# Kernel optimization log

Hardware: AMD Instinct MI355X
Metric: run time of the kernel (lower is better)

## Reference

```python
import jax, jax.numpy as jnp
import numpy as np

NUM_HEADS = 8
KERNEL = 7
LOW_RANK = 4


def setup_inputs() -> dict:
    key = jax.random.key(0)
    ks = jax.random.split(key, 10)
    B, H, W, C = 4, 56, 56, 256
    nh, K, lr = NUM_HEADS, KERNEL, LOW_RANK
    s = 0.02
    return {
        "x": jax.random.normal(ks[0], (B, H, W, C), jnp.float32),
        "Wq": jax.random.normal(ks[1], (C, nh * lr), jnp.float32) * s,
        "bq": jnp.zeros((nh * lr,), jnp.float32),
        "Wk": jax.random.normal(ks[2], (C, nh * lr), jnp.float32) * s,
        "bk": jnp.zeros((nh * lr,), jnp.float32),
        "Wv": jax.random.normal(ks[3], (C, C), jnp.float32) * s,
        "bv": jnp.zeros((C,), jnp.float32),
        "rpb": jax.random.normal(ks[4], (nh, 2 * K - 1, 2 * K - 1), jnp.float32) * s,
        "Wp": jax.random.normal(ks[5], (C, C), jnp.float32) * s,
        "bp": jnp.zeros((C,), jnp.float32),
    }


def reference(x, Wq, bq, Wk, bk, Wv, bv, rpb, Wp, bp):
    B, H, W, C = x.shape
    nh, K, lr = NUM_HEADS, KERNEL, LOW_RANK
    hd = C // nh
    r = K // 2
    scale = hd ** -0.5

    # Projections. Note: the original uses a raw reshape (B,H,W,nh*lr)->(B,nh,H,W,lr),
    # which we replicate exactly (row-major reshape, no permute).
    q = (x @ Wq + bq).reshape(B, nh, H, W, lr) * scale
    k = (x @ Wk + bk).reshape(B, nh, H, W, lr)
    v = (x @ Wv + bv).reshape(B, nh, H, W, hd)

    # NATTEN window start indices (clamped so each query sees exactly K keys per axis).
    start_h = jnp.clip(jnp.arange(H) - r, 0, H - K)  # (H,)
    start_w = jnp.clip(jnp.arange(W) - r, 0, W - K)  # (W,)
    idx_h = start_h[:, None] + jnp.arange(K)[None, :]  # (H, K)
    idx_w = start_w[:, None] + jnp.arange(K)[None, :]  # (W, K)

    # Gather local K/V windows: (B, nh, H, K, W, K, d)
    k_win = k[:, :, idx_h][:, :, :, :, idx_w]
    v_win = v[:, :, idx_h][:, :, :, :, idx_w]

    # Scores: (B, nh, H, W, K, K)
    attn = jnp.einsum('bhijc,bhikjlc->bhijkl', q, k_win)

    # Relative position bias indices: (key_pos - query_pos) + (K-1)
    bi = idx_h - jnp.arange(H)[:, None] + (K - 1)  # (H, K)
    bj = idx_w - jnp.arange(W)[:, None] + (K - 1)  # (W, K)
    bias = rpb[:, bi][:, :, :, bj]                 # (nh, H, K, W, K)
    attn = attn + bias.transpose(0, 1, 3, 2, 4)[None]  # (B, nh, H, W, K, K)

    attn = jax.nn.softmax(attn.reshape(B, nh, H, W, K * K), axis=-1)
    attn = attn.reshape(B, nh, H, W, K, K)

    # Weighted aggregation of V windows: (B, nh, H, W, hd)
    out = jnp.einsum('bhijkl,bhikjld->bhijd', attn, v_win)
    out = out.transpose(0, 2, 3, 1, 4).reshape(B, H, W, C)
    return out @ Wp + bp
```

## Files before the change

### kernel.cpp

```cpp
#include <hip/hip_runtime.h>
#include <hip/hip_bf16.h>

#define BD 4
#define HD_ 56
#define WD 56
#define CD 256
#define NH 8
#define KW 7
#define LR 4
#define HDIM 32
#define MB (HD_*WD)
#define NROWS (BD*MB)
#define QK_PER_B (HD_*WD*32)
#define V_PER_B  (HD_*WD*256)

typedef short short8 __attribute__((ext_vector_type(8)));
typedef float floatx4 __attribute__((ext_vector_type(4)));

static __device__ inline ushort f2bf(float f) {
    __hip_bfloat16 h = __float2bfloat16(f);
    return *(ushort*)&h;
}
static __device__ inline float bf2f(uint h16) {
    union { uint u; float f; } c; c.u = h16 << 16; return c.f;
}
static __device__ inline float bf2f_hi(uint u) {
    union { uint v; float f; } c; c.v = u & 0xffff0000u; return c.f;
}

__global__ __launch_bounds__(256) void prep_all(
    const float* __restrict__ x,
    const float* __restrict__ Wq, const float* __restrict__ Wk,
    const float* __restrict__ Wv, const float* __restrict__ bq,
    const float* __restrict__ bk, const float* __restrict__ bv,
    const float* __restrict__ Wp,
    ushort* __restrict__ Xb, ushort* __restrict__ WpkT,
    ushort* __restrict__ WpT, float* __restrict__ pb)
{
    int blk = blockIdx.x;
    if (blk < 1568) {
        int i8 = (blk * 256 + threadIdx.x) * 8;
        float4 u = *(const float4*)&x[i8];
        float4 v = *(const float4*)&x[i8 + 4];
        union { ushort h[8]; uint4 q; } pk;
        pk.h[0] = f2bf(u.x); pk.h[1] = f2bf(u.y); pk.h[2] = f2bf(u.z); pk.h[3] = f2bf(u.w);
        pk.h[4] = f2bf(v.x); pk.h[5] = f2bf(v.y); pk.h[6] = f2bf(v.z); pk.h[7] = f2bf(v.w);
        *(uint4*)&Xb[i8] = pk.q;
    } else {
        int idx = (blk - 1568) * 256 + threadIdx.x;
        if (idx < 81920) {
            int n = idx >> 8, k = idx & 255;
            float v;
            if (n < 32)       v = Wq[k * 32 + n];
            else if (n < 64)  v = Wk[k * 32 + (n - 32)];
            else              v = Wv[k * 256 + (n - 64)];
            WpkT[idx] = f2bf(v);
        } else if (idx < 81920 + 65536) {
            int j = idx - 81920;
            int n = j >> 8, k = j & 255;
            WpT[j] = f2bf(Wp[k * 256 + n]);
        } else if (idx < 81920 + 65536 + 320) {
            int n = idx - (81920 + 65536);
            pb[n] = (n < 32) ? bq[n] : (n < 64) ? bk[n - 32] : bv[n - 64];
        }
    }
}

__global__ __launch_bounds__(256) void mfma_qkv(
    const ushort* __restrict__ Ag, const ushort* __restrict__ Bt,
    const float* __restrict__ pb, ushort* __restrict__ Qb,
    ushort* __restrict__ Kb, ushort* __restrict__ Vb)
{
    __shared__ ushort As[64 * 40];
    __shared__ ushort Bs[64 * 40];

    const int t = threadIdx.x;
    const int m0 = blockIdx.y * 64;
    const int n0 = blockIdx.x * 64;
    const int r  = t >> 2;
    const int kq = (t & 3) << 3;
    const int lane = t & 63, w = t >> 6;
    const int col = lane & 15, quad = lane >> 4;
    const int q8 = quad << 3;

    floatx4 acc[4] = {{0,0,0,0},{0,0,0,0},{0,0,0,0},{0,0,0,0}};

    for (int k0 = 0; k0 < 256; k0 += 32) {
        uint4 av = *(const uint4*)&Ag[(m0 + r) * 256 + k0 + kq];
        uint4 bv = *(const uint4*)&Bt[(n0 + r) * 256 + k0 + kq];
        __syncthreads();
        *(uint4*)&As[r * 40 + kq] = av;
        *(uint4*)&Bs[r * 40 + kq] = bv;
        __syncthreads();
        short8 af = *(short8*)&As[((w << 4) + col) * 40 + q8];
#pragma unroll
        for (int nt = 0; nt < 4; ++nt) {
            short8 bf = *(short8*)&Bs[((nt << 4) + col) * 40 + q8];
            acc[nt] = __builtin_amdgcn_mfma_f32_16x16x32_bf16(af, bf, acc[nt], 0, 0, 0);
        }
    }

#pragma unroll
    for (int nt = 0; nt < 4; ++nt) {
        int gn = n0 + (nt << 4) + col;
        float bias = pb[gn];
#pragma unroll
        for (int rg = 0; rg < 4; ++rg) {
            int m = m0 + (w << 4) + (quad << 2) + rg;
            ushort h = f2bf(acc[nt][rg] + bias);
            if (n0 == 0 && nt < 2)      Qb[m * 32 + gn] = h;
            else if (n0 == 0)           Kb[m * 32 + (gn - 32)] = h;
            else                        Vb[m * 256 + (gn - 64)] = h;
        }
    }
}

__global__ __launch_bounds__(256) void mfma_out(
    const ushort* __restrict__ Ag, const ushort* __restrict__ Bt,
    const float* __restrict__ bp, float* __restrict__ out)
{
    __shared__ ushort As[64 * 40];
    __shared__ ushort Bs[64 * 40];

    const int t = threadIdx.x;
    const int m0 = blockIdx.y * 64;
    const int n0 = blockIdx.x * 64;
    const int r  = t >> 2;
    const int kq = (t & 3) << 3;
    const int lane = t & 63, w = t >> 6;
    const int col = lane & 15, quad = lane >> 4;
    const int q8 = quad << 3;

    floatx4 acc[4] = {{0,0,0,0},{0,0,0,0},{0,0,0,0},{0,0,0,0}};

    for (int k0 = 0; k0 < 256; k0 += 32) {
        uint4 av = *(const uint4*)&Ag[(m0 + r) * 256 + k0 + kq];
        uint4 bv = *(const uint4*)&Bt[(n0 + r) * 256 + k0 + kq];
        __syncthreads();
        *(uint4*)&As[r * 40 + kq] = av;
        *(uint4*)&Bs[r * 40 + kq] = bv;
        __syncthreads();
        short8 af = *(short8*)&As[((w << 4) + col) * 40 + q8];
#pragma unroll
        for (int nt = 0; nt < 4; ++nt) {
            short8 bf = *(short8*)&Bs[((nt << 4) + col) * 40 + q8];
            acc[nt] = __builtin_amdgcn_mfma_f32_16x16x32_bf16(af, bf, acc[nt], 0, 0, 0);
        }
    }

#pragma unroll
    for (int nt = 0; nt < 4; ++nt) {
        int gn = n0 + (nt << 4) + col;
        float bias = bp[gn];
#pragma unroll
        for (int rg = 0; rg < 4; ++rg) {
            int m = m0 + (w << 4) + (quad << 2) + rg;
            out[m * 256 + gn] = acc[nt][rg] + bias;
        }
    }
}

__global__ __launch_bounds__(256, 8) void natten_attn_t(
    const ushort* __restrict__ Qb, const ushort* __restrict__ Kb,
    const ushort* __restrict__ Vb, const float* __restrict__ rpb,
    ushort* __restrict__ Ab)
{
    __shared__ ushort Ks[196 * 4];
    __shared__ ushort Vs[4 * 196 * 8];
    __shared__ float  Rs[169];

    const int tj = blockIdx.x, ti = blockIdx.y;
    const int n = blockIdx.z & 7, b = blockIdx.z >> 3;
    const int t = threadIdx.x;
    const int i0 = ti * 8, j0 = tj * 8;
    const int rs = min(max(i0 - 3, 0), HD_ - 14);
    const int cs = min(max(j0 - 3, 0), WD - 14);

    const ushort* kb = Kb + b * QK_PER_B + n * (HD_ * WD * LR);
    const ushort* vb = Vb + b * V_PER_B + n * (HD_ * WD * HDIM);

    if (t < 196) {
        int r = t / 14, c = t % 14;
        *(uint2*)&Ks[t * 4] = *(const uint2*)&kb[(rs + r) * (WD * LR) + (cs + c) * LR];
    }
    if (t < 169) Rs[t] = rpb[n * 169 + t];
    for (int idx = t; idx < 784; idx += 256) {
        int oct = idx & 3, pos = idx >> 2;
        int r = pos / 14, c = pos % 14;
        *(uint4*)&Vs[(oct * 196 + pos) * 8] =
            *(const uint4*)&vb[(rs + r) * (WD * HDIM) + (cs + c) * HDIM + oct * 8];
    }
    __syncthreads();

    const int q  = t >> 2, p = t & 3;
    const int qi = q >> 3, qj = q & 7;
    const int i = i0 + qi, j = j0 + qj;
    const int sh = min(max(i - 3, 0), HD_ - KW);
    const int sw = min(max(j - 3, 0), WD - KW);
    const int oh = sh - rs, ow = sw - cs;

    union { uint2 u; uint w[2]; } qr;
    qr.u = *(const uint2*)&Qb[b * QK_PER_B + n * (HD_ * WD * LR) + i * (WD * LR) + j * LR];
    const float scale = 0.17677669529663687f;
    float qx = bf2f(qr.w[0] & 0xffff) * scale, qy = bf2f_hi(qr.w[0]) * scale;
    float qz = bf2f(qr.w[1] & 0xffff) * scale, qw = bf2f_hi(qr.w[1]) * scale;

    const int rb0 = (sh - i + 6) * 13 + (sw - j + 6);

    float mx = -3.4e38f;
    for (int kh = 0; kh < KW; ++kh) {
        int kpos  = (oh + kh) * 14 + ow;
        int rbase = rb0 + kh * 13;
#pragma unroll
        for (int kw = 0; kw < KW; ++kw) {
            union { uint2 u; uint w[2]; } kr;
            kr.u = *(const uint2*)&Ks[(kpos + kw) * 4];
            float d = Rs[rbase + kw];
            d = fmaf(qx, bf2f(kr.w[0] & 0xffff), d);
            d = fmaf(qy, bf2f_hi(kr.w[0]), d);
            d = fmaf(qz, bf2f(kr.w[1] & 0xffff), d);
            d = fmaf(qw, bf2f_hi(kr.w[1]), d);
            mx = fmaxf(mx, d);
        }
    }

    float sum = 0.f;
    float a[8] = {0.f, 0.f, 0.f, 0.f, 0.f, 0.f, 0.f, 0.f};
    const ushort* vsl = &Vs[p * (196 * 8)];
    for (int kh = 0; kh < KW; ++kh) {
        int kpos  = (oh + kh) * 14 + ow;
        int rbase = rb0 + kh * 13;
#pragma unroll
        for (int kw = 0; kw < KW; ++kw) {
            union { uint2 u; uint w[2]; } kr;
            kr.u = *(const uint2*)&Ks[(kpos + kw) * 4];
            float d = Rs[rbase + kw];
            d = fmaf(qx, bf2f(kr.w[0] & 0xffff), d);
            d = fmaf(qy, bf2f_hi(kr.w[0]), d);
            d = fmaf(qz, bf2f(kr.w[1] & 0xffff), d);
            d = fmaf(qw, bf2f_hi(kr.w[1]), d);
            float e = __expf(d - mx);
            sum += e;
            union { uint4 u; uint w[4]; } vr;
            vr.u = *(const uint4*)&vsl[(kpos + kw) * 8];
#pragma unroll
            for (int c = 0; c < 4; ++c) {
                a[2 * c]     = fmaf(e, bf2f(vr.w[c] & 0xffff), a[2 * c]);
                a[2 * c + 1] = fmaf(e, bf2f_hi(vr.w[c]),       a[2 * c + 1]);
            }
        }
    }
    float inv = 1.0f / sum;

    union { ushort h[8]; uint4 u; } pk;
#pragma unroll
    for (int c = 0; c < 8; ++c) pk.h[c] = f2bf(a[c] * inv);
    *(uint4*)&Ab[(((b * HD_ + i) * WD + j)) * CD + n * HDIM + p * 8] = pk.u;
}

extern "C" void kernel_launch(void* const* d_in, const int* in_sizes, int n_in,
                              void* d_out, int out_size, void* d_ws, size_t ws_size,
                              hipStream_t stream) {
    const float* x   = (const float*)d_in[0];
    const float* Wq  = (const float*)d_in[1];
    const float* bq  = (const float*)d_in[2];
    const float* Wk  = (const float*)d_in[3];
    const float* bk  = (const float*)d_in[4];
    const float* Wv  = (const float*)d_in[5];
    const float* bv  = (const float*)d_in[6];
    const float* rpb = (const float*)d_in[7];
    const float* Wp  = (const float*)d_in[8];
    const float* bp  = (const float*)d_in[9];
    float* out = (float*)d_out;

    ushort* WpkT = (ushort*)d_ws;
    ushort* WpT  = WpkT + 81920;
    ushort* Xb   = WpT + 65536;
    ushort* Ab   = Xb + 3211264;
    ushort* Qb   = Ab + 3211264;
    ushort* Kb   = Qb + BD * QK_PER_B;
    ushort* Vb   = Kb + BD * QK_PER_B;
    float*  pb   = (float*)(Vb + BD * V_PER_B);

    prep_all<<<1568 + 578, 256, 0, stream>>>(
        x, Wq, Wk, Wv, bq, bk, bv, Wp, Xb, WpkT, WpT, pb);

    mfma_qkv<<<dim3(5, NROWS / 64), 256, 0, stream>>>(Xb, WpkT, pb, Qb, Kb, Vb);

    natten_attn_t<<<dim3(7, 7, 32), 256, 0, stream>>>(Qb, Kb, Vb, rpb, Ab);

    mfma_out<<<dim3(4, NROWS / 64), 256, 0, stream>>>(Ab, WpT, bp, out);
}
```

Before: 123.3 us.

## Fuse fp32-to-bf16 conversion and weight transpose into the GEMM kernels

After: 129.8 us. 5.3% more time.

```diff
diff --git a/kernel.cpp b/kernel.cpp
--- a/kernel.cpp
+++ b/kernel.cpp
@@ -28,48 +28,12 @@
     union { uint v; float f; } c; c.v = u & 0xffff0000u; return c.f;
 }
 
-__global__ __launch_bounds__(256) void prep_all(
-    const float* __restrict__ x,
+__global__ __launch_bounds__(256) void mfma_qkv(
+    const float* __restrict__ X,
     const float* __restrict__ Wq, const float* __restrict__ Wk,
     const float* __restrict__ Wv, const float* __restrict__ bq,
     const float* __restrict__ bk, const float* __restrict__ bv,
-    const float* __restrict__ Wp,
-    ushort* __restrict__ Xb, ushort* __restrict__ WpkT,
-    ushort* __restrict__ WpT, float* __restrict__ pb)
-{
-    int blk = blockIdx.x;
-    if (blk < 1568) {
-        int i8 = (blk * 256 + threadIdx.x) * 8;
-        float4 u = *(const float4*)&x[i8];
-        float4 v = *(const float4*)&x[i8 + 4];
-        union { ushort h[8]; uint4 q; } pk;
-        pk.h[0] = f2bf(u.x); pk.h[1] = f2bf(u.y); pk.h[2] = f2bf(u.z); pk.h[3] = f2bf(u.w);
-        pk.h[4] = f2bf(v.x); pk.h[5] = f2bf(v.y); pk.h[6] = f2bf(v.z); pk.h[7] = f2bf(v.w);
-        *(uint4*)&Xb[i8] = pk.q;
-    } else {
-        int idx = (blk - 1568) * 256 + threadIdx.x;
-        if (idx < 81920) {
-            int n = idx >> 8, k = idx & 255;
-            float v;
-            if (n < 32)       v = Wq[k * 32 + n];
-            else if (n < 64)  v = Wk[k * 32 + (n - 32)];
-            else              v = Wv[k * 256 + (n - 64)];
-            WpkT[idx] = f2bf(v);
-        } else if (idx < 81920 + 65536) {
-            int j = idx - 81920;
-            int n = j >> 8, k = j & 255;
-            WpT[j] = f2bf(Wp[k * 256 + n]);
-        } else if (idx < 81920 + 65536 + 320) {
-            int n = idx - (81920 + 65536);
-            pb[n] = (n < 32) ? bq[n] : (n < 64) ? bk[n - 32] : bv[n - 64];
-        }
-    }
-}
-
-__global__ __launch_bounds__(256) void mfma_qkv(
-    const ushort* __restrict__ Ag, const ushort* __restrict__ Bt,
-    const float* __restrict__ pb, ushort* __restrict__ Qb,
-    ushort* __restrict__ Kb, ushort* __restrict__ Vb)
+    ushort* __restrict__ Qb, ushort* __restrict__ Kb, ushort* __restrict__ Vb)
 {
     __shared__ ushort As[64 * 40];
     __shared__ ushort Bs[64 * 40];
@@ -83,14 +47,35 @@
     const int col = lane & 15, quad = lane >> 4;
     const int q8 = quad << 3;
 
+    const float* bsrc; int bstride;
+    {
+        int gn = n0 + r;
+        if (gn < 32)      { bsrc = Wq + gn;        bstride = 32;  }
+        else if (gn < 64) { bsrc = Wk + (gn - 32); bstride = 32;  }
+        else              { bsrc = Wv + (gn - 64); bstride = 256; }
+    }
+
     floatx4 acc[4] = {{0,0,0,0},{0,0,0,0},{0,0,0,0},{0,0,0,0}};
 
     for (int k0 = 0; k0 < 256; k0 += 32) {
-        uint4 av = *(const uint4*)&Ag[(m0 + r) * 256 + k0 + kq];
-        uint4 bv = *(const uint4*)&Bt[(n0 + r) * 256 + k0 + kq];
-        __syncthreads();
-        *(uint4*)&As[r * 40 + kq] = av;
-        *(uint4*)&Bs[r * 40 + kq] = bv;
+        float4 a0 = *(const float4*)&X[(m0 + r) * 256 + k0 + kq];
+        float4 a1 = *(const float4*)&X[(m0 + r) * 256 + k0 + kq + 4];
+        float wv0 = bsrc[(k0 + kq + 0) * bstride];
+        float wv1 = bsrc[(k0 + kq + 1) * bstride];
+        float wv2 = bsrc[(k0 + kq + 2) * bstride];
+        float wv3 = bsrc[(k0 + kq + 3) * bstride];
+        float wv4 = bsrc[(k0 + kq + 4) * bstride];
+        float wv5 = bsrc[(k0 + kq + 5) * bstride];
+        float wv6 = bsrc[(k0 + kq + 6) * bstride];
+        float wv7 = bsrc[(k0 + kq + 7) * bstride];
+        union { ushort h[8]; uint4 u; } pa, pb_;
+        pa.h[0] = f2bf(a0.x); pa.h[1] = f2bf(a0.y); pa.h[2] = f2bf(a0.z); pa.h[3] = f2bf(a0.w);
+        pa.h[4] = f2bf(a1.x); pa.h[5] = f2bf(a1.y); pa.h[6] = f2bf(a1.z); pa.h[7] = f2bf(a1.w);
+        pb_.h[0] = f2bf(wv0); pb_.h[1] = f2bf(wv1); pb_.h[2] = f2bf(wv2); pb_.h[3] = f2bf(wv3);
+        pb_.h[4] = f2bf(wv4); pb_.h[5] = f2bf(wv5); pb_.h[6] = f2bf(wv6); pb_.h[7] = f2bf(wv7);
+        __syncthreads();
+        *(uint4*)&As[r * 40 + kq] = pa.u;
+        *(uint4*)&Bs[r * 40 + kq] = pb_.u;
         __syncthreads();
         short8 af = *(short8*)&As[((w << 4) + col) * 40 + q8];
 #pragma unroll
@@ -103,7 +88,7 @@
 #pragma unroll
     for (int nt = 0; nt < 4; ++nt) {
         int gn = n0 + (nt << 4) + col;
-        float bias = pb[gn];
+        float bias = (gn < 32) ? bq[gn] : (gn < 64) ? bk[gn - 32] : bv[gn - 64];
 #pragma unroll
         for (int rg = 0; rg < 4; ++rg) {
             int m = m0 + (w << 4) + (quad << 2) + rg;
@@ -116,7 +101,7 @@
 }
 
 __global__ __launch_bounds__(256) void mfma_out(
-    const ushort* __restrict__ Ag, const ushort* __restrict__ Bt,
+    const ushort* __restrict__ Ag, const float* __restrict__ Wp,
     const float* __restrict__ bp, float* __restrict__ out)
 {
     __shared__ ushort As[64 * 40];
@@ -131,14 +116,26 @@
     const int col = lane & 15, quad = lane >> 4;
     const int q8 = quad << 3;
 
+    const float* bsrc = Wp + (n0 + r);
+
     floatx4 acc[4] = {{0,0,0,0},{0,0,0,0},{0,0,0,0},{0,0,0,0}};
 
     for (int k0 = 0; k0 < 256; k0 += 32) {
         uint4 av = *(const uint4*)&Ag[(m0 + r) * 256 + k0 + kq];
-        uint4 bv = *(const uint4*)&Bt[(n0 + r) * 256 + k0 + kq];
+        float wv0 = bsrc[(k0 + kq + 0) * 256];
+        float wv1 = bsrc[(k0 + kq + 1) * 256];
+        float wv2 = bsrc[(k0 + kq + 2) * 256];
+        float wv3 = bsrc[(k0 + kq + 3) * 256];
+        float wv4 = bsrc[(k0 + kq + 4) * 256];
+        float wv5 = bsrc[(k0 + kq + 5) * 256];
+        float wv6 = bsrc[(k0 + kq + 6) * 256];
+        float wv7 = bsrc[(k0 + kq + 7) * 256];
+        union { ushort h[8]; uint4 u; } pb_;
+        pb_.h[0] = f2bf(wv0); pb_.h[1] = f2bf(wv1); pb_.h[2] = f2bf(wv2); pb_.h[3] = f2bf(wv3);
+        pb_.h[4] = f2bf(wv4); pb_.h[5] = f2bf(wv5); pb_.h[6] = f2bf(wv6); pb_.h[7] = f2bf(wv7);
         __syncthreads();
         *(uint4*)&As[r * 40 + kq] = av;
-        *(uint4*)&Bs[r * 40 + kq] = bv;
+        *(uint4*)&Bs[r * 40 + kq] = pb_.u;
         __syncthreads();
         short8 af = *(short8*)&As[((w << 4) + col) * 40 + q8];
 #pragma unroll
@@ -273,21 +270,15 @@
     const float* bp  = (const float*)d_in[9];
     float* out = (float*)d_out;
 
-    ushort* WpkT = (ushort*)d_ws;
-    ushort* WpT  = WpkT + 81920;
-    ushort* Xb   = WpT + 65536;
-    ushort* Ab   = Xb + 3211264;
-    ushort* Qb   = Ab + 3211264;
-    ushort* Kb   = Qb + BD * QK_PER_B;
-    ushort* Vb   = Kb + BD * QK_PER_B;
-    float*  pb   = (float*)(Vb + BD * V_PER_B);
-
-    prep_all<<<1568 + 578, 256, 0, stream>>>(
-        x, Wq, Wk, Wv, bq, bk, bv, Wp, Xb, WpkT, WpT, pb);
-
-    mfma_qkv<<<dim3(5, NROWS / 64), 256, 0, stream>>>(Xb, WpkT, pb, Qb, Kb, Vb);
+    ushort* Ab = (ushort*)d_ws;
+    ushort* Qb = Ab + 3211264;
+    ushort* Kb = Qb + BD * QK_PER_B;
+    ushort* Vb = Kb + BD * QK_PER_B;
+
+    mfma_qkv<<<dim3(5, NROWS / 64), 256, 0, stream>>>(
+        x, Wq, Wk, Wv, bq, bk, bv, Qb, Kb, Vb);
 
     natten_attn_t<<<dim3(7, 7, 32), 256, 0, stream>>>(Qb, Kb, Vb, rpb, Ab);
 
-    mfma_out<<<dim3(4, NROWS / 64), 256, 0, stream>>>(Ab, WpT, bp, out);
-}
+    mfma_out<<<dim3(4, NROWS / 64), 256, 0, stream>>>(Ab, Wp, bp, out);
+}
```
